# Kernel tuning notes

Measured on AMD Instinct MI355X. Metric: run time of the kernel, lower is better.

The kernel has to match this reference:

```python
import jax, jax.numpy as jnp
import numpy as np

K = 16
EPS = 1e-5
NEG_SLOPE = 0.2


def leaky(x):
    return jnp.where(x > 0, x, NEG_SLOPE * x)


def batchnorm_train(x, gamma, beta):
    # x: [B, D]; training-mode BN with biased variance (torch semantics)
    mean = jnp.mean(x, axis=0)
    var = jnp.mean((x - mean) ** 2, axis=0)
    return (x - mean) * jax.lax.rsqrt(var + EPS) * gamma + beta


def setup_inputs() -> dict:
    key = jax.random.key(0)
    ks = jax.random.split(key, 20)
    N, M, D = 30000, 8000, 16
    s = lambda fan_in: 1.0 / np.sqrt(fan_in)
    inp = {
        "xyz": jax.random.normal(ks[0], (N, 3), jnp.float32),
        "atom_xyz": jax.random.normal(ks[1], (M, 3), jnp.float32),
        "atom_types": jax.random.normal(ks[2], (M, D), jnp.float32),
        "Wt1": jax.random.uniform(ks[3], (D, D), jnp.float32, -s(D), s(D)),
        "bt1": jax.random.uniform(ks[4], (D,), jnp.float32, -s(D), s(D)),
        "Wt2": jax.random.uniform(ks[5], (D, D), jnp.float32, -s(D), s(D)),
        "bt2": jax.random.uniform(ks[6], (D,), jnp.float32, -s(D), s(D)),
        "Wt3": jax.random.uniform(ks[7], (D, D), jnp.float32, -s(D), s(D)),
        "bt3": jax.random.uniform(ks[8], (D,), jnp.float32, -s(D), s(D)),
        # embed: conv1 Linear(D+1, D), conv2 Linear(D, D), conv3 Linear(2D, D)
        "W1": jax.random.uniform(ks[9], (D + 1, D), jnp.float32, -s(D + 1), s(D + 1)),
        "b1": jax.random.uniform(ks[10], (D,), jnp.float32, -s(D + 1), s(D + 1)),
        "W2": jax.random.uniform(ks[11], (D, D), jnp.float32, -s(D), s(D)),
        "b2": jax.random.uniform(ks[12], (D,), jnp.float32, -s(D), s(D)),
        "W3": jax.random.uniform(ks[13], (2 * D, D), jnp.float32, -s(2 * D), s(2 * D)),
        "b3": jax.random.uniform(ks[14], (D,), jnp.float32, -s(2 * D), s(2 * D)),
        # batchnorm affine params
        "g1": jnp.ones((D,), jnp.float32),
        "be1": jnp.zeros((D,), jnp.float32),
        "g2": jnp.ones((D,), jnp.float32),
        "be2": jnp.zeros((D,), jnp.float32),
    }
    return inp


def reference(xyz, atom_xyz, atom_types,
              Wt1, bt1, Wt2, bt2, Wt3, bt3,
              W1, b1, W2, b2, W3, b3, g1, be1, g2, be2):
    N, D = xyz.shape[0], atom_types.shape[1]

    # transform_types MLP on atom features: [M, D]
    t = leaky(atom_types @ Wt1 + bt1)
    t = leaky(t @ Wt2 + bt2)
    t = leaky(t @ Wt3 + bt3)

    # kNN: squared distances via GEMM expansion (avoids [N,M,3])
    d2 = (jnp.sum(xyz ** 2, axis=1, keepdims=True)
          + jnp.sum(atom_xyz ** 2, axis=1)[None, :]
          - 2.0 * xyz @ atom_xyz.T)                      # [N, M]
    _, idx = jax.lax.top_k(-d2, K)                       # [N, K] nearest atoms

    # gather neighbor coords, recompute exact squared dists (as in source)
    y_ik = atom_xyz[idx]                                 # [N, K, 3]
    dists = jnp.sum((xyz[:, None, :] - y_ik) ** 2, axis=-1)  # [N, K]

    feat = jnp.concatenate([t[idx], (1.0 / dists)[..., None]], axis=-1)  # [N,K,D+1]

    # conv1 -> leaky -> bn1 -> sum-pool
    fx = feat @ W1 + b1                                  # [N, K, D]
    fx = batchnorm_train(leaky(fx).reshape(-1, D), g1, be1).reshape(N, K, D)
    fx1 = fx.sum(axis=1)                                 # [N, D]

    # conv2 -> leaky -> bn2 -> sum-pool
    fx = fx @ W2 + b2
    fx = batchnorm_train(leaky(fx).reshape(-1, D), g2, be2).reshape(N, K, D)
    fx2 = fx.sum(axis=1)                                 # [N, D]

    return jnp.concatenate([fx1, fx2], axis=-1) @ W3 + b3  # [N, D]
```

## Files before the change

kernel.cpp:

```cpp
#include <hip/hip_runtime.h>

#define N_PTS   30000
#define M_ATOMS 8000
#define D       16
#define KNN     16
#define NGRP    125
#define EPS     1e-5f
#define SLOPE   0.2f
#define BN_COUNT 480000.0f

typedef unsigned long long ull;

__device__ __forceinline__ float leaky(float x) { return x > 0.f ? x : SLOPE * x; }

__device__ __forceinline__ unsigned fkey(float f) {
  unsigned u = __float_as_uint(f);
  return u ^ ((u & 0x80000000u) ? 0xFFFFFFFFu : 0x80000000u);
}

#define DPPSTEP32(v, CTRL) {                                                   \
  unsigned t_ = (unsigned)__builtin_amdgcn_update_dpp(-1, (int)(v), CTRL, 0xF, 0xF, false); \
  (v) = t_ < (v) ? t_ : (v); }

__device__ __forceinline__ unsigned wmin32d(unsigned v) {
  DPPSTEP32(v, 0x111); DPPSTEP32(v, 0x112); DPPSTEP32(v, 0x114);
  DPPSTEP32(v, 0x118); DPPSTEP32(v, 0x142); DPPSTEP32(v, 0x143);
  return (unsigned)__builtin_amdgcn_readlane((int)v, 63);
}

#define DPPSTEP64(lo, hi, CTRL) {                                              \
  unsigned tlo_ = (unsigned)__builtin_amdgcn_update_dpp(-1, (int)(lo), CTRL, 0xF, 0xF, false); \
  unsigned thi_ = (unsigned)__builtin_amdgcn_update_dpp(-1, (int)(hi), CTRL, 0xF, 0xF, false); \
  bool lt_ = (thi_ < (hi)) || ((thi_ == (hi)) && (tlo_ < (lo)));               \
  (lo) = lt_ ? tlo_ : (lo); (hi) = lt_ ? thi_ : (hi); }

__device__ __forceinline__ ull wmin64d(ull v) {
  unsigned lo = (unsigned)v, hi = (unsigned)(v >> 32);
  DPPSTEP64(lo, hi, 0x111); DPPSTEP64(lo, hi, 0x112); DPPSTEP64(lo, hi, 0x114);
  DPPSTEP64(lo, hi, 0x118); DPPSTEP64(lo, hi, 0x142); DPPSTEP64(lo, hi, 0x143);
  unsigned flo = (unsigned)__builtin_amdgcn_readlane((int)lo, 63);
  unsigned fhi = (unsigned)__builtin_amdgcn_readlane((int)hi, 63);
  return ((ull)fhi << 32) | flo;
}

__device__ __forceinline__ void cswap(ull& a, ull& b) {
  ull mn = a < b ? a : b, mx = a < b ? b : a;
  a = mn; b = mx;
}

#define LAYER(IN, OUT, W, B)                                        \
  _Pragma("unroll") for (int j = 0; j < 16; ++j) {                  \
    float acc = B[j];                                               \
    _Pragma("unroll") for (int i = 0; i < 16; ++i)                  \
      acc = fmaf(IN[i], W[i*16+j], acc);                            \
    OUT[j] = leaky(acc);                                            \
  }

__global__ void __launch_bounds__(256) k1_prep(
    const float* __restrict__ atom_xyz, const float* __restrict__ atom_types,
    const float* __restrict__ Wt1, const float* __restrict__ bt1,
    const float* __restrict__ Wt2, const float* __restrict__ bt2,
    const float* __restrict__ Wt3, const float* __restrict__ bt3,
    const float* __restrict__ W1, const float* __restrict__ b1,
    float4* __restrict__ atoms4, float* __restrict__ tu_out,
    float* __restrict__ gstats) {
  __shared__ float w1[256], w2[256], w3[256], wc[256];
  __shared__ float bb1[16], bb2[16], bb3[16], bbc[16];
  int tid = threadIdx.x;
  if (blockIdx.x == 0 && tid < 64) gstats[tid] = 0.f;
  w1[tid] = Wt1[tid]; w2[tid] = Wt2[tid]; w3[tid] = Wt3[tid]; wc[tid] = W1[tid];
  if (tid < 16) { bb1[tid] = bt1[tid]; bb2[tid] = bt2[tid]; bb3[tid] = bt3[tid]; bbc[tid] = b1[tid]; }
  __syncthreads();
  int m = blockIdx.x * 256 + tid;
  if (m >= M_ATOMS) return;
  float ax = atom_xyz[m*3+0], ay = atom_xyz[m*3+1], az = atom_xyz[m*3+2];
  atoms4[m] = make_float4(ax, ay, az, fmaf(ax,ax, fmaf(ay,ay, az*az)));

  float u[16], v[16];
  const float4* tp = (const float4*)(atom_types + (size_t)m*16);
  float4 q0 = tp[0], q1 = tp[1], q2 = tp[2], q3 = tp[3];
  u[0]=q0.x; u[1]=q0.y; u[2]=q0.z; u[3]=q0.w;
  u[4]=q1.x; u[5]=q1.y; u[6]=q1.z; u[7]=q1.w;
  u[8]=q2.x; u[9]=q2.y; u[10]=q2.z; u[11]=q2.w;
  u[12]=q3.x; u[13]=q3.y; u[14]=q3.z; u[15]=q3.w;

  LAYER(u, v, w1, bb1);
  LAYER(v, u, w2, bb2);
  LAYER(u, v, w3, bb3);
  float up[16];
#pragma unroll
  for (int j = 0; j < 16; ++j) {
    float acc = bbc[j];
#pragma unroll
    for (int i = 0; i < 16; ++i) acc = fmaf(v[i], wc[i*16+j], acc);
    up[j] = acc;
  }

  float4* op = (float4*)(tu_out + (size_t)m*16);
  op[0] = make_float4(up[0], up[1], up[2], up[3]);
  op[1] = make_float4(up[4], up[5], up[6], up[7]);
  op[2] = make_float4(up[8], up[9], up[10], up[11]);
  op[3] = make_float4(up[12], up[13], up[14], up[15]);
}

__global__ void __launch_bounds__(1024) k_sort(
    const float4* __restrict__ atoms4, float4* __restrict__ atoms4s,
    int* __restrict__ origid) {
  __shared__ int h0[4096], h1[4096];
  int tid = threadIdx.x;
  for (int i = tid; i < 4096; i += 1024) h0[i] = 0;
  __syncthreads();
  int mycell[8];
#pragma unroll
  for (int r = 0; r < 8; ++r) {
    int m = r*1024 + tid;
    if (m < M_ATOMS) {
      float4 a = atoms4[m];
      int cx = min(max((int)floorf((a.x + 4.f) * 2.f), 0), 15);
      int cy = min(max((int)floorf((a.y + 4.f) * 2.f), 0), 15);
      int cz = min(max((int)floorf((a.z + 4.f) * 2.f), 0), 15);
      int c = 0;
#pragma unroll
      for (int b = 0; b < 4; ++b)
        c |= (((cx>>b)&1) << (3*b)) | (((cy>>b)&1) << (3*b+1)) | (((cz>>b)&1) << (3*b+2));
      mycell[r] = c;
      atomicAdd(&h0[c], 1);
    } else mycell[r] = -1;
  }
  __syncthreads();
  int* src = h0; int* dst = h1;
  for (int off = 1; off < 4096; off <<= 1) {
    for (int i = tid; i < 4096; i += 1024) {
      int v = src[i];
      if (i >= off) v += src[i-off];
      dst[i] = v;
    }
    __syncthreads();
    int* tswap = src; src = dst; dst = tswap;
  }
  for (int i = tid; i < 4096; i += 1024) dst[i] = (i == 0) ? 0 : src[i-1];
  __syncthreads();
#pragma unroll
  for (int r = 0; r < 8; ++r) {
    int m = r*1024 + tid;
    if (m < M_ATOMS) {
      int pos = atomicAdd(&dst[mycell[r]], 1);
      atoms4s[pos] = atoms4[m];
      origid[pos] = m;
    }
  }
}

__global__ void __launch_bounds__(256) k_bounds(
    const float4* __restrict__ atoms4s, float4* __restrict__ bounds) {
  int lane = threadIdx.x & 63;
  int g = blockIdx.x * 4 + (threadIdx.x >> 6);
  if (g >= NGRP) return;
  float4 a = atoms4s[(g << 6) + lane];
  float mnx=a.x, mny=a.y, mnz=a.z, mxx=a.x, mxy=a.y, mxz=a.z;
#pragma unroll
  for (int off = 32; off; off >>= 1) {
    mnx = fminf(mnx, __shfl_xor(mnx, off, 64));
    mny = fminf(mny, __shfl_xor(mny, off, 64));
    mnz = fminf(mnz, __shfl_xor(mnz, off, 64));
    mxx = fmaxf(mxx, __shfl_xor(mxx, off, 64));
    mxy = fmaxf(mxy, __shfl_xor(mxy, off, 64));
    mxz = fmaxf(mxz, __shfl_xor(mxz, off, 64));
  }
  if (lane == 0) {
    bounds[2*g]   = make_float4(mnx, mny, mnz, 0.f);
    bounds[2*g+1] = make_float4(mxx, mxy, mxz, 0.f);
  }
}

__global__ void __launch_bounds__(256) k2_knn(
    const float* __restrict__ xyz, const float4* __restrict__ atoms4s,
    const int* __restrict__ origid, const float4* __restrict__ bounds,
    const float* __restrict__ atom_xyz,
    int2* __restrict__ pairs) {
  int lane = threadIdx.x & 63;
  int n = blockIdx.x * 4 + (threadIdx.x >> 6);
  if (n >= N_PTS) return;

  float px = xyz[n*3+0], py = xyz[n*3+1], pz = xyz[n*3+2];
  float x2 = fmaf(px,px, fmaf(py,py, pz*pz));

  unsigned ea, eb = 0xFFFFFFFFu;
  {
    int g = lane;
    float4 mn = bounds[2*g], mx = bounds[2*g+1];
    float dx = fmaxf(fmaxf(mn.x - px, px - mx.x), 0.f);
    float dy = fmaxf(fmaxf(mn.y - py, py - mx.y), 0.f);
    float dz = fmaxf(fmaxf(mn.z - pz, pz - mx.z), 0.f);
    float lb = fmaf(dx,dx, fmaf(dy,dy, dz*dz)) * 0.999f - 1e-4f;
    ea = (fkey(lb) & 0xFFFFFF00u) | (unsigned)g;
  }
  if (lane + 64 < NGRP) {
    int g = lane + 64;
    float4 mn = bounds[2*g], mx = bounds[2*g+1];
    float dx = fmaxf(fmaxf(mn.x - px, px - mx.x), 0.f);
    float dy = fmaxf(fmaxf(mn.y - py, py - mx.y), 0.f);
    float dz = fmaxf(fmaxf(mn.z - pz, pz - mx.z), 0.f);
    float lb = fmaf(dx,dx, fmaf(dy,dy, dz*dz)) * 0.999f - 1e-4f;
    eb = (fkey(lb) & 0xFFFFFF00u) | (unsigned)g;
  }
  unsigned cur = ea < eb ? ea : eb;
  unsigned bak = ea < eb ? eb : ea;

  int gs[4];
#pragma unroll
  for (int r = 0; r < 4; ++r) {
    unsigned m = wmin32d(cur);
    bool own = (cur == m);
    cur = own ? bak : cur;
    bak = own ? 0xFFFFFFFFu : bak;
    gs[r] = (int)(m & 0xFFu);
  }

  float4 A[4]; int OI[4];
#pragma unroll
  for (int r = 0; r < 4; ++r) {
    int base = gs[r] << 6;
    A[r]  = atoms4s[base + lane];
    OI[r] = origid [base + lane];
  }
  ull E[4];
#pragma unroll
  for (int r = 0; r < 4; ++r) {
    float dotp = fmaf(px,A[r].x, fmaf(py,A[r].y, pz*A[r].z));
    float d2 = (x2 + A[r].w) - 2.f*dotp;
    E[r] = ((ull)fkey(d2) << 32) | (unsigned)OI[r];
  }
  cswap(E[0],E[1]); cswap(E[2],E[3]); cswap(E[0],E[2]);
  cswap(E[1],E[3]); cswap(E[1],E[2]);

  ull c64 = E[0], l1 = E[1], l2 = E[2], l3 = E[3];
  ull res = ~0ull, m64 = 0;
#pragma unroll
  for (int r = 0; r < KNN; ++r) {
    m64 = wmin64d(c64);
    if (lane == r) res = m64;
    bool own = (c64 == m64);
    c64 = own ? l1 : c64;
    l1  = own ? l2 : l1;
    l2  = own ? l3 : l2;
    l3  = own ? ~0ull : l3;
  }
  ull lv = res;
  ull thresh = m64;

  for (int it = 0; it < NGRP - 4; ++it) {
    unsigned m = wmin32d(cur);
    if ((m & 0xFFFFFF00u) >= (unsigned)(thresh >> 32)) break;
    bool own = (cur == m);
    cur = own ? bak : cur;
    bak = own ? 0xFFFFFFFFu : bak;
    int base = (int)(m & 0xFFu) << 6;

    float4 a = atoms4s[base + lane];
    int oi = origid[base + lane];
    float dotp = fmaf(px,a.x, fmaf(py,a.y, pz*a.z));
    float d2 = (x2 + a.w) - 2.f*dotp;
    ull key = ((ull)fkey(d2) << 32) | (unsigned)oi;

    ull mk = __ballot(key < thresh);
    while (mk) {
      int src = (int)(__ffsll(mk) - 1);
      mk &= mk - 1;
      unsigned klo = (unsigned)__builtin_amdgcn_readlane((int)(unsigned)key, src);
      unsigned khi = (unsigned)__builtin_amdgcn_readlane((int)(unsigned)(key >> 32), src);
      ull kc = ((ull)khi << 32) | klo;
      if (kc < thresh) {
        bool ins = (lane < KNN) && (kc < lv);
        unsigned pvlo = (unsigned)__builtin_amdgcn_update_dpp(0, (int)(unsigned)lv,        0x111, 0xF, 0xF, false);
        unsigned pvhi = (unsigned)__builtin_amdgcn_update_dpp(0, (int)(unsigned)(lv>>32), 0x111, 0xF, 0xF, false);
        int pins      =           __builtin_amdgcn_update_dpp(0, ins ? 1 : 0,              0x111, 0xF, 0xF, false);
        if (ins) lv = pins ? (((ull)pvhi << 32) | pvlo) : kc;
        unsigned tlo = (unsigned)__builtin_amdgcn_readlane((int)(unsigned)lv, KNN-1);
        unsigned thi = (unsigned)__builtin_amdgcn_readlane((int)(unsigned)(lv >> 32), KNN-1);
        thresh = ((ull)thi << 32) | tlo;
      }
    }
  }

  if (lane < KNN) {
    int oi = (int)(unsigned)(lv & 0xFFFFFFFFull);
    float bx = atom_xyz[oi*3+0], by = atom_xyz[oi*3+1], bz = atom_xyz[oi*3+2];
    float dx = px - bx, dy = py - by, dz = pz - bz;
    float dd = fmaf(dx,dx, fmaf(dy,dy, dz*dz));
    pairs[n*KNN + lane] = make_int2(oi, __float_as_int(1.f / dd));
  }
}

__device__ __forceinline__ void a1_row(const float* __restrict__ tu, int idx,
                                       float iv, const float* wiv, float* a) {
  const float4* up = (const float4*)(tu + (size_t)idx*16);
  float4 r0 = up[0], r1 = up[1], r2 = up[2], r3 = up[3];
  float u[16];
  u[0]=r0.x; u[1]=r0.y; u[2]=r0.z; u[3]=r0.w;
  u[4]=r1.x; u[5]=r1.y; u[6]=r1.z; u[7]=r1.w;
  u[8]=r2.x; u[9]=r2.y; u[10]=r2.z; u[11]=r2.w;
  u[12]=r3.x; u[13]=r3.y; u[14]=r3.z; u[15]=r3.w;
#pragma unroll
  for (int j = 0; j < 16; ++j) a[j] = leaky(fmaf(iv, wiv[j], u[j]));
}

__global__ void __launch_bounds__(256, 6) k3_stats1(
    const int2* __restrict__ pairs, const float* __restrict__ tu,
    const float* __restrict__ W1, float* __restrict__ gstats) {
  __shared__ float wiv[16];
  __shared__ float buf[16*16*17];
  int tid = threadIdx.x;
  if (tid < 16) wiv[tid] = W1[256 + tid];
  __syncthreads();

  int g = blockIdx.x * 256 + tid;
  int p = tid >> 4, k = tid & 15;
  int2 pr = pairs[g];
  int idx = pr.x;
  float iv = __int_as_float(pr.y);
  float a[16];
  a1_row(tu, idx, iv, wiv, a);

  float* myrow = &buf[(p*16 + k)*17];
  int p2 = tid >> 4, j2 = tid & 15;
#pragma unroll
  for (int j = 0; j < 16; ++j) myrow[j] = a[j];
  __syncthreads();
  float s = 0.f;
#pragma unroll
  for (int kk = 0; kk < 16; ++kk) s += buf[(p2*16+kk)*17 + j2];
  __syncthreads();
#pragma unroll
  for (int j = 0; j < 16; ++j) myrow[j] = a[j]*a[j];
  __syncthreads();
  float q = 0.f;
#pragma unroll
  for (int kk = 0; kk < 16; ++kk) q += buf[(p2*16+kk)*17 + j2];
  __syncthreads();
  buf[p2*17 + j2] = s;
  buf[289 + p2*17 + j2] = q;
  __syncthreads();
  if (tid < 16) {
    float t1 = 0.f, t2 = 0.f;
#pragma unroll
    for (int pp = 0; pp < 16; ++pp) { t1 += buf[pp*17 + tid]; t2 += buf[289 + pp*17 + tid]; }
    atomicAdd(&gstats[tid],      t1);
    atomicAdd(&gstats[16 + tid], t2);
  }
}

__global__ void __launch_bounds__(256, 4) k4_main(
    const int2* __restrict__ pairs, const float* __restrict__ tu,
    const float* __restrict__ W1,
    const float* __restrict__ W2, const float* __restrict__ b2,
    const float* __restrict__ g1, const float* __restrict__ be1,
    float* __restrict__ fx1_out, float* __restrict__ s2_out,
    float* __restrict__ gstats) {
  __shared__ float wiv[16], w2s[256], b2s[16];
  __shared__ float sc1[16], sh1[16];
  __shared__ float buf[16*16*17];
  int tid = threadIdx.x;
  w2s[tid] = W2[tid];
  if (tid < 16) { wiv[tid] = W1[256 + tid]; b2s[tid] = b2[tid]; }
  if (tid < 16) {
    float mean = gstats[tid]    * (1.f/BN_COUNT);
    float var  = gstats[16+tid] * (1.f/BN_COUNT) - mean*mean;
    float sC = g1[tid] / sqrtf(var + EPS);
    sc1[tid] = sC;
    sh1[tid] = be1[tid] - mean * sC;
  }
  __syncthreads();

  int g = blockIdx.x * 256 + tid;
  int p = tid >> 4, k = tid & 15;
  int2 pr = pairs[g];
  int idx = pr.x;
  float iv = __int_as_float(pr.y);
  float h[16], a2[16];
  a1_row(tu, idx, iv, wiv, h);
#pragma unroll
  for (int j = 0; j < 16; ++j) h[j] = fmaf(h[j], sc1[j], sh1[j]);
#pragma unroll
  for (int j = 0; j < 16; ++j) {
    float accj = b2s[j];
#pragma unroll
    for (int i = 0; i < 16; ++i) accj = fmaf(h[i], w2s[i*16+j], accj);
    a2[j] = leaky(accj);
  }

  float* myrow = &buf[(p*16 + k)*17];
  int p2 = tid >> 4, j2 = tid & 15;
#pragma unroll
  for (int j = 0; j < 16; ++j) myrow[j] = h[j];
  __syncthreads();
  {
    float s = 0.f;
#pragma unroll
    for (int kk = 0; kk < 16; ++kk) s += buf[(p2*16+kk)*17 + j2];
    fx1_out[(size_t)blockIdx.x*256 + tid] = s;
  }
  __syncthreads();
#pragma unroll
  for (int j = 0; j < 16; ++j) myrow[j] = a2[j];
  __syncthreads();
  float s2v = 0.f;
#pragma unroll
  for (int kk = 0; kk < 16; ++kk) s2v += buf[(p2*16+kk)*17 + j2];
  s2_out[(size_t)blockIdx.x*256 + tid] = s2v;
  __syncthreads();
#pragma unroll
  for (int j = 0; j < 16; ++j) myrow[j] = a2[j]*a2[j];
  __syncthreads();
  float q2v = 0.f;
#pragma unroll
  for (int kk = 0; kk < 16; ++kk) q2v += buf[(p2*16+kk)*17 + j2];
  __syncthreads();
  buf[p2*17 + j2] = s2v;
  buf[289 + p2*17 + j2] = q2v;
  __syncthreads();
  if (tid < 16) {
    float t1 = 0.f, t2 = 0.f;
#pragma unroll
    for (int pp = 0; pp < 16; ++pp) { t1 += buf[pp*17 + tid]; t2 += buf[289 + pp*17 + tid]; }
    atomicAdd(&gstats[32 + tid], t1);
    atomicAdd(&gstats[48 + tid], t2);
  }
}

__global__ void __launch_bounds__(256) k5_final(
    const float* __restrict__ fx1_in, const float* __restrict__ s2_in,
    const float* __restrict__ gstats,
    const float* __restrict__ W3, const float* __restrict__ b3,
    const float* __restrict__ g2, const float* __restrict__ be2,
    float* __restrict__ out) {
  __shared__ float w[512], bb[16], sc2[16], sh2[16];
  int tid = threadIdx.x;
  w[tid] = W3[tid]; w[256+tid] = W3[256+tid];
  if (tid < 16) {
    bb[tid] = b3[tid];
    float mean = gstats[32+tid] * (1.f/BN_COUNT);
    float var  = gstats[48+tid] * (1.f/BN_COUNT) - mean*mean;
    float s = g2[tid] / sqrtf(var + EPS);
    sc2[tid] = s;
    sh2[tid] = be2[tid] - mean * s;
  }
  __syncthreads();
  int n = blockIdx.x * 256 + tid;
  if (n >= N_PTS) return;

  const float4* f1p = (const float4*)(fx1_in + (size_t)n*16);
  const float4* f2p = (const float4*)(s2_in  + (size_t)n*16);
  float4 x0=f1p[0], x1=f1p[1], x2=f1p[2], x3=f1p[3];
  float4 y0=f2p[0], y1=f2p[1], y2=f2p[2], y3=f2p[3];
  float f1[16] = {x0.x,x0.y,x0.z,x0.w, x1.x,x1.y,x1.z,x1.w,
                  x2.x,x2.y,x2.z,x2.w, x3.x,x3.y,x3.z,x3.w};
  float f2[16] = {y0.x,y0.y,y0.z,y0.w, y1.x,y1.y,y1.z,y1.w,
                  y2.x,y2.y,y2.z,y2.w, y3.x,y3.y,y3.z,y3.w};
#pragma unroll
  for (int i = 0; i < 16; ++i) f2[i] = fmaf(sc2[i], f2[i], 16.f * sh2[i]);

  float4* op = (float4*)(out + (size_t)n*16);
  float o[16];
#pragma unroll
  for (int j = 0; j < 16; ++j) {
    float accj = bb[j];
#pragma unroll
    for (int i = 0; i < 16; ++i) accj = fmaf(f1[i], w[i*16+j], accj);
#pragma unroll
    for (int i = 0; i < 16; ++i) accj = fmaf(f2[i], w[(16+i)*16+j], accj);
    o[j] = accj;
  }
  op[0] = make_float4(o[0], o[1], o[2], o[3]);
  op[1] = make_float4(o[4], o[5], o[6], o[7]);
  op[2] = make_float4(o[8], o[9], o[10], o[11]);
  op[3] = make_float4(o[12], o[13], o[14], o[15]);
}

extern "C" void kernel_launch(void* const* d_in, const int* in_sizes, int n_in,
                              void* d_out, int out_size, void* d_ws, size_t ws_size,
                              hipStream_t stream) {
  const float* xyz        = (const float*)d_in[0];
  const float* atom_xyz   = (const float*)d_in[1];
  const float* atom_types = (const float*)d_in[2];
  const float* Wt1 = (const float*)d_in[3];  const float* bt1 = (const float*)d_in[4];
  const float* Wt2 = (const float*)d_in[5];  const float* bt2 = (const float*)d_in[6];
  const float* Wt3 = (const float*)d_in[7];  const float* bt3 = (const float*)d_in[8];
  const float* W1  = (const float*)d_in[9];  const float* b1  = (const float*)d_in[10];
  const float* W2  = (const float*)d_in[11]; const float* b2  = (const float*)d_in[12];
  const float* W3  = (const float*)d_in[13]; const float* b3  = (const float*)d_in[14];
  const float* g1  = (const float*)d_in[15]; const float* be1 = (const float*)d_in[16];
  const float* g2  = (const float*)d_in[17]; const float* be2 = (const float*)d_in[18];
  float* out = (float*)d_out;

  float* ws = (float*)d_ws;
  float4* atoms4   = (float4*)ws;
  float*  tu       = ws + 32256;
  int2*   pairs    = (int2*)(ws + 160256);
  float*  fx1      = ws + 1120256;
  float*  s2       = ws + 1600256;
  float*  gstats   = ws + 2080256;
  float4* atoms4s  = (float4*)(ws + 1120256);
  int*    origid   = (int*)(ws + 1152256);
  float4* bounds   = (float4*)(ws + 1160256);

  k1_prep<<<32, 256, 0, stream>>>(atom_xyz, atom_types, Wt1, bt1, Wt2, bt2,
                                  Wt3, bt3, W1, b1, atoms4, tu, gstats);
  k_sort<<<1, 1024, 0, stream>>>(atoms4, atoms4s, origid);
  k_bounds<<<32, 256, 0, stream>>>(atoms4s, bounds);
  k2_knn<<<7500, 256, 0, stream>>>(xyz, atoms4s, origid, bounds, atom_xyz, pairs);
  k3_stats1<<<1875, 256, 0, stream>>>(pairs, tu, W1, gstats);
  k4_main<<<1875, 256, 0, stream>>>(pairs, tu, W1, W2, b2, g1, be1,
                                    fx1, s2, gstats);
  k5_final<<<118, 256, 0, stream>>>(fx1, s2, gstats, W3, b3, g2, be2, out);
}
```

Before: 262.7 us.

## Fuse atom prep, sort and bounds; fold BN1 stats into kNN kernel

Atom preprocessing, Morton counting sort and group bounding boxes now run in one launch. Block 0 does the sort and computes bounds with shared-memory atomic min/max on order-preserving keys, while the other blocks run the type MLP. The first-layer batchnorm statistics are now accumulated at the end of the kNN kernel, which removes the separate stats pass that re-read pairs and gathered features, and the atomics go to 8 partial buckets to reduce contention. The 64-bit DPP wave-min in the kNN seeding is replaced by a 32-bit min plus a ballot tie-break, at the cost of a serial single-block sort, a longer kNN kernel and extra gathers inside it.

```diff
diff --git a/kernel.cpp b/kernel.cpp
--- a/kernel.cpp
+++ b/kernel.cpp
@@ -17,6 +17,10 @@
   unsigned u = __float_as_uint(f);
   return u ^ ((u & 0x80000000u) ? 0xFFFFFFFFu : 0x80000000u);
 }
+__device__ __forceinline__ float unfkey(unsigned e) {
+  unsigned u = (e & 0x80000000u) ? (e ^ 0x80000000u) : ~e;
+  return __uint_as_float(u);
+}
 
 #define DPPSTEP32(v, CTRL) {                                                   \
   unsigned t_ = (unsigned)__builtin_amdgcn_update_dpp(-1, (int)(v), CTRL, 0xF, 0xF, false); \
@@ -28,24 +32,20 @@
   return (unsigned)__builtin_amdgcn_readlane((int)v, 63);
 }
 
-#define DPPSTEP64(lo, hi, CTRL) {                                              \
-  unsigned tlo_ = (unsigned)__builtin_amdgcn_update_dpp(-1, (int)(lo), CTRL, 0xF, 0xF, false); \
-  unsigned thi_ = (unsigned)__builtin_amdgcn_update_dpp(-1, (int)(hi), CTRL, 0xF, 0xF, false); \
-  bool lt_ = (thi_ < (hi)) || ((thi_ == (hi)) && (tlo_ < (lo)));               \
-  (lo) = lt_ ? tlo_ : (lo); (hi) = lt_ ? thi_ : (hi); }
-
-__device__ __forceinline__ ull wmin64d(ull v) {
-  unsigned lo = (unsigned)v, hi = (unsigned)(v >> 32);
-  DPPSTEP64(lo, hi, 0x111); DPPSTEP64(lo, hi, 0x112); DPPSTEP64(lo, hi, 0x114);
-  DPPSTEP64(lo, hi, 0x118); DPPSTEP64(lo, hi, 0x142); DPPSTEP64(lo, hi, 0x143);
-  unsigned flo = (unsigned)__builtin_amdgcn_readlane((int)lo, 63);
-  unsigned fhi = (unsigned)__builtin_amdgcn_readlane((int)hi, 63);
-  return ((ull)fhi << 32) | flo;
-}
-
 __device__ __forceinline__ void cswap(ull& a, ull& b) {
   ull mn = a < b ? a : b, mx = a < b ? b : a;
   a = mn; b = mx;
+}
+
+__device__ __forceinline__ int morton_cell(float x, float y, float z) {
+  int cx = min(max((int)floorf((x + 4.f) * 2.f), 0), 15);
+  int cy = min(max((int)floorf((y + 4.f) * 2.f), 0), 15);
+  int cz = min(max((int)floorf((z + 4.f) * 2.f), 0), 15);
+  int c = 0;
+#pragma unroll
+  for (int b = 0; b < 4; ++b)
+    c |= (((cx>>b)&1) << (3*b)) | (((cy>>b)&1) << (3*b+1)) | (((cz>>b)&1) << (3*b+2));
+  return c;
 }
 
 #define LAYER(IN, OUT, W, B)                                        \
@@ -56,131 +56,110 @@
     OUT[j] = leaky(acc);                                            \
   }
 
-__global__ void __launch_bounds__(256) k1_prep(
+__global__ void __launch_bounds__(256) kA_prep(
     const float* __restrict__ atom_xyz, const float* __restrict__ atom_types,
     const float* __restrict__ Wt1, const float* __restrict__ bt1,
     const float* __restrict__ Wt2, const float* __restrict__ bt2,
     const float* __restrict__ Wt3, const float* __restrict__ bt3,
     const float* __restrict__ W1, const float* __restrict__ b1,
-    float4* __restrict__ atoms4, float* __restrict__ tu_out,
+    float* __restrict__ tu_out, float4* __restrict__ atoms4s,
+    int* __restrict__ origid, float4* __restrict__ bounds,
     float* __restrict__ gstats) {
-  __shared__ float w1[256], w2[256], w3[256], wc[256];
-  __shared__ float bb1[16], bb2[16], bb3[16], bbc[16];
   int tid = threadIdx.x;
-  if (blockIdx.x == 0 && tid < 64) gstats[tid] = 0.f;
-  w1[tid] = Wt1[tid]; w2[tid] = Wt2[tid]; w3[tid] = Wt3[tid]; wc[tid] = W1[tid];
-  if (tid < 16) { bb1[tid] = bt1[tid]; bb2[tid] = bt2[tid]; bb3[tid] = bt3[tid]; bbc[tid] = b1[tid]; }
-  __syncthreads();
-  int m = blockIdx.x * 256 + tid;
-  if (m >= M_ATOMS) return;
-  float ax = atom_xyz[m*3+0], ay = atom_xyz[m*3+1], az = atom_xyz[m*3+2];
-  atoms4[m] = make_float4(ax, ay, az, fmaf(ax,ax, fmaf(ay,ay, az*az)));
-
-  float u[16], v[16];
-  const float4* tp = (const float4*)(atom_types + (size_t)m*16);
-  float4 q0 = tp[0], q1 = tp[1], q2 = tp[2], q3 = tp[3];
-  u[0]=q0.x; u[1]=q0.y; u[2]=q0.z; u[3]=q0.w;
-  u[4]=q1.x; u[5]=q1.y; u[6]=q1.z; u[7]=q1.w;
-  u[8]=q2.x; u[9]=q2.y; u[10]=q2.z; u[11]=q2.w;
-  u[12]=q3.x; u[13]=q3.y; u[14]=q3.z; u[15]=q3.w;
-
-  LAYER(u, v, w1, bb1);
-  LAYER(v, u, w2, bb2);
-  LAYER(u, v, w3, bb3);
-  float up[16];
-#pragma unroll
-  for (int j = 0; j < 16; ++j) {
-    float acc = bbc[j];
-#pragma unroll
-    for (int i = 0; i < 16; ++i) acc = fmaf(v[i], wc[i*16+j], acc);
-    up[j] = acc;
-  }
-
-  float4* op = (float4*)(tu_out + (size_t)m*16);
-  op[0] = make_float4(up[0], up[1], up[2], up[3]);
-  op[1] = make_float4(up[4], up[5], up[6], up[7]);
-  op[2] = make_float4(up[8], up[9], up[10], up[11]);
-  op[3] = make_float4(up[12], up[13], up[14], up[15]);
-}
-
-__global__ void __launch_bounds__(1024) k_sort(
-    const float4* __restrict__ atoms4, float4* __restrict__ atoms4s,
-    int* __restrict__ origid) {
-  __shared__ int h0[4096], h1[4096];
-  int tid = threadIdx.x;
-  for (int i = tid; i < 4096; i += 1024) h0[i] = 0;
-  __syncthreads();
-  int mycell[8];
-#pragma unroll
-  for (int r = 0; r < 8; ++r) {
-    int m = r*1024 + tid;
-    if (m < M_ATOMS) {
-      float4 a = atoms4[m];
-      int cx = min(max((int)floorf((a.x + 4.f) * 2.f), 0), 15);
-      int cy = min(max((int)floorf((a.y + 4.f) * 2.f), 0), 15);
-      int cz = min(max((int)floorf((a.z + 4.f) * 2.f), 0), 15);
-      int c = 0;
-#pragma unroll
-      for (int b = 0; b < 4; ++b)
-        c |= (((cx>>b)&1) << (3*b)) | (((cy>>b)&1) << (3*b+1)) | (((cz>>b)&1) << (3*b+2));
-      mycell[r] = c;
-      atomicAdd(&h0[c], 1);
-    } else mycell[r] = -1;
-  }
-  __syncthreads();
-  int* src = h0; int* dst = h1;
-  for (int off = 1; off < 4096; off <<= 1) {
-    for (int i = tid; i < 4096; i += 1024) {
-      int v = src[i];
-      if (i >= off) v += src[i-off];
-      dst[i] = v;
-    }
+  if (blockIdx.x == 0) {
+    __shared__ int h0[4096], h1[4096];
+    __shared__ unsigned bmn[375], bmx[375];
+    for (int i = tid; i < 4096; i += 256) { h0[i] = 0; }
+    for (int i = tid; i < 375; i += 256) { bmn[i] = 0xFFFFFFFFu; bmx[i] = 0u; }
+    for (int i = tid; i < 288; i += 256) gstats[i] = 0.f;
     __syncthreads();
-    int* tswap = src; src = dst; dst = tswap;
-  }
-  for (int i = tid; i < 4096; i += 1024) dst[i] = (i == 0) ? 0 : src[i-1];
-  __syncthreads();
-#pragma unroll
-  for (int r = 0; r < 8; ++r) {
-    int m = r*1024 + tid;
-    if (m < M_ATOMS) {
-      int pos = atomicAdd(&dst[mycell[r]], 1);
-      atoms4s[pos] = atoms4[m];
-      origid[pos] = m;
-    }
-  }
-}
-
-__global__ void __launch_bounds__(256) k_bounds(
-    const float4* __restrict__ atoms4s, float4* __restrict__ bounds) {
-  int lane = threadIdx.x & 63;
-  int g = blockIdx.x * 4 + (threadIdx.x >> 6);
-  if (g >= NGRP) return;
-  float4 a = atoms4s[(g << 6) + lane];
-  float mnx=a.x, mny=a.y, mnz=a.z, mxx=a.x, mxy=a.y, mxz=a.z;
-#pragma unroll
-  for (int off = 32; off; off >>= 1) {
-    mnx = fminf(mnx, __shfl_xor(mnx, off, 64));
-    mny = fminf(mny, __shfl_xor(mny, off, 64));
-    mnz = fminf(mnz, __shfl_xor(mnz, off, 64));
-    mxx = fmaxf(mxx, __shfl_xor(mxx, off, 64));
-    mxy = fmaxf(mxy, __shfl_xor(mxy, off, 64));
-    mxz = fmaxf(mxz, __shfl_xor(mxz, off, 64));
-  }
-  if (lane == 0) {
-    bounds[2*g]   = make_float4(mnx, mny, mnz, 0.f);
-    bounds[2*g+1] = make_float4(mxx, mxy, mxz, 0.f);
+    for (int r = 0; r < 32; ++r) {
+      int m = r*256 + tid;
+      if (m < M_ATOMS) {
+        int c = morton_cell(atom_xyz[m*3], atom_xyz[m*3+1], atom_xyz[m*3+2]);
+        atomicAdd(&h0[c], 1);
+      }
+    }
+    __syncthreads();
+    int* src = h0; int* dst = h1;
+    for (int off = 1; off < 4096; off <<= 1) {
+      for (int i = tid; i < 4096; i += 256) {
+        int v = src[i];
+        if (i >= off) v += src[i-off];
+        dst[i] = v;
+      }
+      __syncthreads();
+      int* t = src; src = dst; dst = t;
+    }
+    for (int i = tid; i < 4096; i += 256) dst[i] = i ? src[i-1] : 0;
+    __syncthreads();
+    for (int r = 0; r < 32; ++r) {
+      int m = r*256 + tid;
+      if (m < M_ATOMS) {
+        float x = atom_xyz[m*3], y = atom_xyz[m*3+1], z = atom_xyz[m*3+2];
+        int c = morton_cell(x, y, z);
+        int pos = atomicAdd(&dst[c], 1);
+        atoms4s[pos] = make_float4(x, y, z, fmaf(x,x, fmaf(y,y, z*z)));
+        origid[pos] = m;
+        int g = pos >> 6;
+        atomicMin(&bmn[g],     fkey(x)); atomicMax(&bmx[g],     fkey(x));
+        atomicMin(&bmn[125+g], fkey(y)); atomicMax(&bmx[125+g], fkey(y));
+        atomicMin(&bmn[250+g], fkey(z)); atomicMax(&bmx[250+g], fkey(z));
+      }
+    }
+    __syncthreads();
+    if (tid < NGRP) {
+      bounds[2*tid]   = make_float4(unfkey(bmn[tid]), unfkey(bmn[125+tid]),
+                                    unfkey(bmn[250+tid]), 0.f);
+      bounds[2*tid+1] = make_float4(unfkey(bmx[tid]), unfkey(bmx[125+tid]),
+                                    unfkey(bmx[250+tid]), 0.f);
+    }
+  } else {
+    __shared__ float w1[256], w2[256], w3[256], wc[256];
+    __shared__ float bb1[16], bb2[16], bb3[16], bbc[16];
+    w1[tid] = Wt1[tid]; w2[tid] = Wt2[tid]; w3[tid] = Wt3[tid]; wc[tid] = W1[tid];
+    if (tid < 16) { bb1[tid] = bt1[tid]; bb2[tid] = bt2[tid];
+                    bb3[tid] = bt3[tid]; bbc[tid] = b1[tid]; }
+    __syncthreads();
+    int m = (blockIdx.x - 1) * 256 + tid;
+    if (m >= M_ATOMS) return;
+    float u[16], v[16];
+    const float4* tp = (const float4*)(atom_types + (size_t)m*16);
+    float4 q0 = tp[0], q1 = tp[1], q2 = tp[2], q3 = tp[3];
+    u[0]=q0.x; u[1]=q0.y; u[2]=q0.z; u[3]=q0.w;
+    u[4]=q1.x; u[5]=q1.y; u[6]=q1.z; u[7]=q1.w;
+    u[8]=q2.x; u[9]=q2.y; u[10]=q2.z; u[11]=q2.w;
+    u[12]=q3.x; u[13]=q3.y; u[14]=q3.z; u[15]=q3.w;
+    LAYER(u, v, w1, bb1);
+    LAYER(v, u, w2, bb2);
+    LAYER(u, v, w3, bb3);
+    float up[16];
+#pragma unroll
+    for (int j = 0; j < 16; ++j) {
+      float acc = bbc[j];
+#pragma unroll
+      for (int i = 0; i < 16; ++i) acc = fmaf(v[i], wc[i*16+j], acc);
+      up[j] = acc;
+    }
+    float4* op = (float4*)(tu_out + (size_t)m*16);
+    op[0] = make_float4(up[0], up[1], up[2], up[3]);
+    op[1] = make_float4(up[4], up[5], up[6], up[7]);
+    op[2] = make_float4(up[8], up[9], up[10], up[11]);
+    op[3] = make_float4(up[12], up[13], up[14], up[15]);
   }
 }
 
 __global__ void __launch_bounds__(256) k2_knn(
     const float* __restrict__ xyz, const float4* __restrict__ atoms4s,
     const int* __restrict__ origid, const float4* __restrict__ bounds,
-    const float* __restrict__ atom_xyz,
-    int2* __restrict__ pairs) {
-  int lane = threadIdx.x & 63;
-  int n = blockIdx.x * 4 + (threadIdx.x >> 6);
-  if (n >= N_PTS) return;
+    const float* __restrict__ atom_xyz, const float* __restrict__ tu,
+    const float* __restrict__ W1,
+    int2* __restrict__ pairs, float* __restrict__ gstats) {
+  __shared__ float sbuf[4*16*20];
+  int tid = threadIdx.x;
+  int lane = tid & 63;
+  int wid = tid >> 6;
+  int n = blockIdx.x * 4 + wid;
 
   float px = xyz[n*3+0], py = xyz[n*3+1], pz = xyz[n*3+2];
   float x2 = fmaf(px,px, fmaf(py,py, pz*pz));
@@ -233,21 +212,32 @@
   }
   cswap(E[0],E[1]); cswap(E[2],E[3]); cswap(E[0],E[2]);
   cswap(E[1],E[3]); cswap(E[1],E[2]);
-
-  ull c64 = E[0], l1 = E[1], l2 = E[2], l3 = E[3];
-  ull res = ~0ull, m64 = 0;
-#pragma unroll
+  unsigned cf0 = (unsigned)(E[0] >> 32), ci0 = (unsigned)E[0];
+  unsigned cf1 = (unsigned)(E[1] >> 32), ci1 = (unsigned)E[1];
+  unsigned cf2 = (unsigned)(E[2] >> 32), ci2 = (unsigned)E[2];
+  unsigned cf3 = (unsigned)(E[3] >> 32), ci3 = (unsigned)E[3];
+
+  ull res = ~0ull;
+  unsigned mf = 0, mi = 0;
   for (int r = 0; r < KNN; ++r) {
-    m64 = wmin64d(c64);
-    if (lane == r) res = m64;
-    bool own = (c64 == m64);
-    c64 = own ? l1 : c64;
-    l1  = own ? l2 : l1;
-    l2  = own ? l3 : l2;
-    l3  = own ? ~0ull : l3;
+    mf = wmin32d(cf0);
+    ull ball = __ballot(cf0 == mf);
+    if (__popcll(ball) == 1) {
+      int srcl = (int)(__ffsll(ball) - 1);
+      mi = (unsigned)__builtin_amdgcn_readlane((int)ci0, srcl);
+    } else {
+      unsigned cand = (cf0 == mf) ? ci0 : 0xFFFFFFFFu;
+      mi = wmin32d(cand);
+    }
+    bool own = (cf0 == mf) && (ci0 == mi);
+    if (lane == r) res = (((ull)mf) << 32) | mi;
+    cf0 = own ? cf1 : cf0; cf1 = own ? cf2 : cf1;
+    cf2 = own ? cf3 : cf2; cf3 = own ? 0xFFFFFFFFu : cf3;
+    ci0 = own ? ci1 : ci0; ci1 = own ? ci2 : ci1;
+    ci2 = own ? ci3 : ci2; ci3 = own ? 0xFFFFFFFFu : ci3;
   }
   ull lv = res;
-  ull thresh = m64;
+  ull thresh = (((ull)mf) << 32) | mi;
 
   for (int it = 0; it < NGRP - 4; ++it) {
     unsigned m = wmin32d(cur);
@@ -258,10 +248,10 @@
     int base = (int)(m & 0xFFu) << 6;
 
     float4 a = atoms4s[base + lane];
-    int oi = origid[base + lane];
+    int oi2 = origid[base + lane];
     float dotp = fmaf(px,a.x, fmaf(py,a.y, pz*a.z));
     float d2 = (x2 + a.w) - 2.f*dotp;
-    ull key = ((ull)fkey(d2) << 32) | (unsigned)oi;
+    ull key = ((ull)fkey(d2) << 32) | (unsigned)oi2;
 
     ull mk = __ballot(key < thresh);
     while (mk) {
@@ -283,12 +273,53 @@
     }
   }
 
+  int oi = (int)(unsigned)(lv & 0xFFFFFFFFull);
+  float iv = 0.f;
   if (lane < KNN) {
-    int oi = (int)(unsigned)(lv & 0xFFFFFFFFull);
     float bx = atom_xyz[oi*3+0], by = atom_xyz[oi*3+1], bz = atom_xyz[oi*3+2];
     float dx = px - bx, dy = py - by, dz = pz - bz;
     float dd = fmaf(dx,dx, fmaf(dy,dy, dz*dz));
-    pairs[n*KNN + lane] = make_int2(oi, __float_as_int(1.f / dd));
+    iv = 1.f / dd;
+    pairs[n*KNN + lane] = make_int2(oi, __float_as_int(iv));
+
+    const float4* up4 = (const float4*)(tu + (size_t)oi*16);
+    float4 u0 = up4[0], u1 = up4[1], u2 = up4[2], u3 = up4[3];
+    float4* row = (float4*)&sbuf[(wid*16 + lane)*20];
+    float4 w;
+    w.x = leaky(fmaf(iv, W1[256+ 0], u0.x)); w.y = leaky(fmaf(iv, W1[256+ 1], u0.y));
+    w.z = leaky(fmaf(iv, W1[256+ 2], u0.z)); w.w = leaky(fmaf(iv, W1[256+ 3], u0.w));
+    row[0] = w;
+    w.x = leaky(fmaf(iv, W1[256+ 4], u1.x)); w.y = leaky(fmaf(iv, W1[256+ 5], u1.y));
+    w.z = leaky(fmaf(iv, W1[256+ 6], u1.z)); w.w = leaky(fmaf(iv, W1[256+ 7], u1.w));
+    row[1] = w;
+    w.x = leaky(fmaf(iv, W1[256+ 8], u2.x)); w.y = leaky(fmaf(iv, W1[256+ 9], u2.y));
+    w.z = leaky(fmaf(iv, W1[256+10], u2.z)); w.w = leaky(fmaf(iv, W1[256+11], u2.w));
+    row[2] = w;
+    w.x = leaky(fmaf(iv, W1[256+12], u3.x)); w.y = leaky(fmaf(iv, W1[256+13], u3.y));
+    w.z = leaky(fmaf(iv, W1[256+14], u3.z)); w.w = leaky(fmaf(iv, W1[256+15], u3.w));
+    row[3] = w;
+  }
+  __syncthreads();
+  {
+    int ch = tid & 15, grp = tid >> 4;
+    float S = 0.f, Q = 0.f;
+#pragma unroll
+    for (int i = 0; i < 4; ++i) {
+      float v = sbuf[(grp*4 + i)*20 + ch];
+      S += v; Q += v*v;
+    }
+    __syncthreads();
+    sbuf[grp*20 + ch] = S;
+    sbuf[400 + grp*20 + ch] = Q;
+  }
+  __syncthreads();
+  if (tid < 32) {
+    int ch = tid & 15;
+    int off = (tid < 16) ? 0 : 400;
+    float s = 0.f;
+#pragma unroll
+    for (int g = 0; g < 16; ++g) s += sbuf[off + g*20 + ch];
+    atomicAdd(&gstats[(blockIdx.x & 7)*32 + tid], s);
   }
 }
 
@@ -303,51 +334,6 @@
   u[12]=r3.x; u[13]=r3.y; u[14]=r3.z; u[15]=r3.w;
 #pragma unroll
   for (int j = 0; j < 16; ++j) a[j] = leaky(fmaf(iv, wiv[j], u[j]));
-}
-
-__global__ void __launch_bounds__(256, 6) k3_stats1(
-    const int2* __restrict__ pairs, const float* __restrict__ tu,
-    const float* __restrict__ W1, float* __restrict__ gstats) {
-  __shared__ float wiv[16];
-  __shared__ float buf[16*16*17];
-  int tid = threadIdx.x;
-  if (tid < 16) wiv[tid] = W1[256 + tid];
-  __syncthreads();
-
-  int g = blockIdx.x * 256 + tid;
-  int p = tid >> 4, k = tid & 15;
-  int2 pr = pairs[g];
-  int idx = pr.x;
-  float iv = __int_as_float(pr.y);
-  float a[16];
-  a1_row(tu, idx, iv, wiv, a);
-
-  float* myrow = &buf[(p*16 + k)*17];
-  int p2 = tid >> 4, j2 = tid & 15;
-#pragma unroll
-  for (int j = 0; j < 16; ++j) myrow[j] = a[j];
-  __syncthreads();
-  float s = 0.f;
-#pragma unroll
-  for (int kk = 0; kk < 16; ++kk) s += buf[(p2*16+kk)*17 + j2];
-  __syncthreads();
-#pragma unroll
-  for (int j = 0; j < 16; ++j) myrow[j] = a[j]*a[j];
-  __syncthreads();
-  float q = 0.f;
-#pragma unroll
-  for (int kk = 0; kk < 16; ++kk) q += buf[(p2*16+kk)*17 + j2];
-  __syncthreads();
-  buf[p2*17 + j2] = s;
-  buf[289 + p2*17 + j2] = q;
-  __syncthreads();
-  if (tid < 16) {
-    float t1 = 0.f, t2 = 0.f;
-#pragma unroll
-    for (int pp = 0; pp < 16; ++pp) { t1 += buf[pp*17 + tid]; t2 += buf[289 + pp*17 + tid]; }
-    atomicAdd(&gstats[tid],      t1);
-    atomicAdd(&gstats[16 + tid], t2);
-  }
 }
 
 __global__ void __launch_bounds__(256, 4) k4_main(
@@ -364,8 +350,11 @@
   w2s[tid] = W2[tid];
   if (tid < 16) { wiv[tid] = W1[256 + tid]; b2s[tid] = b2[tid]; }
   if (tid < 16) {
-    float mean = gstats[tid]    * (1.f/BN_COUNT);
-    float var  = gstats[16+tid] * (1.f/BN_COUNT) - mean*mean;
+    float s1 = 0.f, q1 = 0.f;
+#pragma unroll
+    for (int c = 0; c < 8; ++c) { s1 += gstats[c*32 + tid]; q1 += gstats[c*32 + 16 + tid]; }
+    float mean = s1 * (1.f/BN_COUNT);
+    float var  = q1 * (1.f/BN_COUNT) - mean*mean;
     float sC = g1[tid] / sqrtf(var + EPS);
     sc1[tid] = sC;
     sh1[tid] = be1[tid] - mean * sC;
@@ -423,8 +412,8 @@
     float t1 = 0.f, t2 = 0.f;
 #pragma unroll
     for (int pp = 0; pp < 16; ++pp) { t1 += buf[pp*17 + tid]; t2 += buf[289 + pp*17 + tid]; }
-    atomicAdd(&gstats[32 + tid], t1);
-    atomicAdd(&gstats[48 + tid], t2);
+    atomicAdd(&gstats[256 + tid], t1);
+    atomicAdd(&gstats[272 + tid], t2);
   }
 }
 
@@ -439,8 +428,8 @@
   w[tid] = W3[tid]; w[256+tid] = W3[256+tid];
   if (tid < 16) {
     bb[tid] = b3[tid];
-    float mean = gstats[32+tid] * (1.f/BN_COUNT);
-    float var  = gstats[48+tid] * (1.f/BN_COUNT) - mean*mean;
+    float mean = gstats[256+tid] * (1.f/BN_COUNT);
+    float var  = gstats[272+tid] * (1.f/BN_COUNT) - mean*mean;
     float s = g2[tid] / sqrtf(var + EPS);
     sc2[tid] = s;
     sh2[tid] = be2[tid] - mean * s;
@@ -494,22 +483,20 @@
   float* out = (float*)d_out;
 
   float* ws = (float*)d_ws;
-  float4* atoms4   = (float4*)ws;
-  float*  tu       = ws + 32256;
-  int2*   pairs    = (int2*)(ws + 160256);
-  float*  fx1      = ws + 1120256;
-  float*  s2       = ws + 1600256;
-  float*  gstats   = ws + 2080256;
-  float4* atoms4s  = (float4*)(ws + 1120256);
-  int*    origid   = (int*)(ws + 1152256);
-  float4* bounds   = (float4*)(ws + 1160256);
-
-  k1_prep<<<32, 256, 0, stream>>>(atom_xyz, atom_types, Wt1, bt1, Wt2, bt2,
-                                  Wt3, bt3, W1, b1, atoms4, tu, gstats);
-  k_sort<<<1, 1024, 0, stream>>>(atoms4, atoms4s, origid);
-  k_bounds<<<32, 256, 0, stream>>>(atoms4s, bounds);
-  k2_knn<<<7500, 256, 0, stream>>>(xyz, atoms4s, origid, bounds, atom_xyz, pairs);
-  k3_stats1<<<1875, 256, 0, stream>>>(pairs, tu, W1, gstats);
+  float*  tu       = ws;
+  int2*   pairs    = (int2*)(ws + 128000);
+  float*  fx1      = ws + 1088000;
+  float*  s2       = ws + 1568000;
+  float*  gstats   = ws + 2048000;
+  float4* atoms4s  = (float4*)(ws + 1088000);
+  int*    origid   = (int*)(ws + 1120000);
+  float4* bounds   = (float4*)(ws + 1128000);
+
+  kA_prep<<<33, 256, 0, stream>>>(atom_xyz, atom_types, Wt1, bt1, Wt2, bt2,
+                                  Wt3, bt3, W1, b1, tu, atoms4s, origid,
+                                  bounds, gstats);
+  k2_knn<<<7500, 256, 0, stream>>>(xyz, atoms4s, origid, bounds, atom_xyz,
+                                   tu, W1, pairs, gstats);
   k4_main<<<1875, 256, 0, stream>>>(pairs, tu, W1, W2, b2, g1, be1,
                                     fx1, s2, gstats);
   k5_final<<<118, 256, 0, stream>>>(fx1, s2, gstats, W3, b3, g2, be2, out);
```

Result: faster. 235.7 us (-10.3%).
